# Kernel tuning notes

Hardware: AMD Instinct MI355X
Metric: run time of the kernel (lower is better)

Reference implementation:

```python
import jax, jax.numpy as jnp
import numpy as np

D_MODEL = 1024
NUM_HEADS = 16
D_K = D_MODEL // NUM_HEADS


def setup_inputs() -> dict:
    key = jax.random.key(0)
    ks = jax.random.split(key, 10)
    s = 1.0 / np.sqrt(D_MODEL)  # ~ torch Linear init scale
    inp = {
        "x": jax.random.normal(ks[0], (2, 2048, D_MODEL), dtype=jnp.float32),
        "Wq": jax.random.uniform(ks[1], (D_MODEL, D_MODEL), jnp.float32, -s, s),
        "bq": jax.random.uniform(ks[2], (D_MODEL,), jnp.float32, -s, s),
        "Wk": jax.random.uniform(ks[3], (D_MODEL, D_MODEL), jnp.float32, -s, s),
        "bk": jax.random.uniform(ks[4], (D_MODEL,), jnp.float32, -s, s),
        "Wv": jax.random.uniform(ks[5], (D_MODEL, D_MODEL), jnp.float32, -s, s),
        "bv": jax.random.uniform(ks[6], (D_MODEL,), jnp.float32, -s, s),
        "Wo": jax.random.uniform(ks[7], (D_MODEL, D_MODEL), jnp.float32, -s, s),
        "bo": jax.random.uniform(ks[8], (D_MODEL,), jnp.float32, -s, s),
        "ln_gamma": jnp.ones((D_MODEL,), jnp.float32),
        "ln_beta": jnp.zeros((D_MODEL,), jnp.float32),
    }
    return inp


def reference(x, Wq, bq, Wk, bk, Wv, bv, Wo, bo, ln_gamma, ln_beta):
    B, S, D = x.shape
    residual = x
    # LayerNorm (eps=1e-5 as torch default)
    mu = jnp.mean(x, axis=-1, keepdims=True)
    var = jnp.mean(jnp.square(x - mu), axis=-1, keepdims=True)
    xn = (x - mu) * jax.lax.rsqrt(var + 1e-5) * ln_gamma + ln_beta
    # QKV projections (torch Linear: y = x @ W^T + b) -> (B, H, S, d_k)
    def proj(W, b):
        return (xn @ W.T + b).reshape(B, S, NUM_HEADS, D_K).transpose(0, 2, 1, 3)
    Q, K, V = proj(Wq, bq), proj(Wk, bk), proj(Wv, bv)
    scores = jnp.einsum("bhqd,bhkd->bhqk", Q, K) / np.sqrt(D_K).astype(np.float32)
    attn = jax.nn.softmax(scores, axis=-1)  # (B, H, S, S); dropout is no-op (eval)
    context = jnp.einsum("bhqk,bhkd->bhqd", attn, V)
    context = context.transpose(0, 2, 1, 3).reshape(B, S, D)
    out = context @ Wo.T + bo
    return out + residual, attn.mean(axis=1)
```

## Files before the change

### kernel.cpp

```cpp
#include <hip/hip_runtime.h>
#include <stdint.h>
#include <stddef.h>

#define DEV static __device__ __forceinline__

typedef float f32x4 __attribute__((ext_vector_type(4)));
typedef float f32x16 __attribute__((ext_vector_type(16)));
typedef unsigned u32x4 __attribute__((ext_vector_type(4)));
typedef __bf16 bf16x8 __attribute__((ext_vector_type(8)));

DEV short f2bf(float f) {
  union { float f; unsigned u; } a; a.f = f;
  unsigned r = a.u + 0x7fffu + ((a.u >> 16) & 1u);
  return (short)(r >> 16);
}

DEV void gld_lds16(const void* g, void* lds) {
  __builtin_amdgcn_global_load_lds(
      (__attribute__((address_space(1))) void*)(void*)g,
      (__attribute__((address_space(3))) void*)lds, 16, 0, 0);
}

DEV f32x4 MFMA(bf16x8 a, bf16x8 b, f32x4 c) {
  return __builtin_amdgcn_mfma_f32_16x16x32_bf16(a, b, c, 0, 0, 0);
}
DEV f32x16 MFMA32(bf16x8 a, bf16x8 b, f32x16 c) {
  return __builtin_amdgcn_mfma_f32_32x32x16_bf16(a, b, c, 0, 0, 0);
}

DEV float ex2(float x) { return __builtin_amdgcn_exp2f(x); }

DEV unsigned cvtpk(float lo, float hi) {
  unsigned r;
  asm("v_cvt_pk_bf16_f32 %0, %1, %2" : "=v"(r) : "v"(lo), "v"(hi));
  return r;
}

DEV float xhalf_sum(float v) {
  float a = v, b = v;
  asm volatile("v_permlane32_swap_b32 %0, %1" : "+v"(a), "+v"(b));
  return a + b;
}

#define LOG2E 1.4426950408889634f


__global__ __launch_bounds__(256) void k_cvtw_ln(
    const float* __restrict__ w0, const float* __restrict__ w1,
    const float* __restrict__ w2, const float* __restrict__ w3,
    short* __restrict__ dst, const float* __restrict__ x,
    const float* __restrict__ g, const float* __restrict__ be,
    short* __restrict__ xn) {
  __shared__ float ps[4], pss[4];
  if (blockIdx.x < 4096) {
    int i = blockIdx.x * 256 + threadIdx.x;
    int sel = i >> 18;
    const float* src = sel == 0 ? w0 : sel == 1 ? w1 : sel == 2 ? w2 : w3;
    int off = (i & 0x3ffff) * 4;
    float4 v = *(const float4*)(src + off);
    short4 o4; o4.x = f2bf(v.x); o4.y = f2bf(v.y); o4.z = f2bf(v.z); o4.w = f2bf(v.w);
    *(short4*)(dst + (size_t)i * 4) = o4;
  } else {
    int row = blockIdx.x - 4096;
    int t = threadIdx.x;
    const float4* xr = (const float4*)(x + (size_t)row * 1024);
    float4 v = xr[t];
    float s = v.x + v.y + v.z + v.w;
    float ss = v.x * v.x + v.y * v.y + v.z * v.z + v.w * v.w;
#pragma unroll
    for (int o = 32; o; o >>= 1) { s += __shfl_down(s, o); ss += __shfl_down(ss, o); }
    int w = t >> 6, lane = t & 63;
    if (lane == 0) { ps[w] = s; pss[w] = ss; }
    __syncthreads();
    float st = ps[0] + ps[1] + ps[2] + ps[3];
    float sst = pss[0] + pss[1] + pss[2] + pss[3];
    float mean = st * (1.0f / 1024.0f);
    float var = sst * (1.0f / 1024.0f) - mean * mean;
    float rstd = rsqrtf(var + 1e-5f);
    float4 gv = ((const float4*)g)[t];
    float4 bv = ((const float4*)be)[t];
    short4 o4;
    o4.x = f2bf((v.x - mean) * rstd * gv.x + bv.x);
    o4.y = f2bf((v.y - mean) * rstd * gv.y + bv.y);
    o4.z = f2bf((v.z - mean) * rstd * gv.z + bv.z);
    o4.w = f2bf((v.w - mean) * rstd * gv.w + bv.w);
    ((short4*)(xn + (size_t)row * 1024))[t] = o4;
  }
}

__global__ __launch_bounds__(256) void k_gemm_qkv(
    const short* __restrict__ xn, const short* __restrict__ wbf,
    const float* __restrict__ bq, const float* __restrict__ bk,
    const float* __restrict__ bv, short* __restrict__ q_ws,
    short* __restrict__ k_ws, short* __restrict__ v_ws) {
  __shared__ __align__(16) short at[128 * 32];
  __shared__ __align__(16) short bt[128 * 32];
  int t = threadIdx.x, lane = t & 63, w = t >> 6;
  int wr = w >> 1, wc = w & 1;
  int z = blockIdx.z;
  int row0 = blockIdx.y * 128, col0 = blockIdx.x * 128;
  const short* A = xn + (size_t)row0 * 1024;
  const short* Bw = wbf + (size_t)z * (1024 * 1024) + (size_t)col0 * 1024;
  f32x4 acc[4][4];
#pragma unroll
  for (int m = 0; m < 4; m++)
#pragma unroll
    for (int n = 0; n < 4; n++) acc[m][n] = (f32x4)0.0f;

  for (int k0 = 0; k0 < 1024; k0 += 32) {
#pragma unroll
    for (int i = 0; i < 2; i++) {
      int c = t + i * 256;
      int r = c >> 2, cc = (c & 3) * 8;
      gld_lds16(A + (size_t)r * 1024 + k0 + cc, &at[c * 8]);
      gld_lds16(Bw + (size_t)r * 1024 + k0 + cc, &bt[c * 8]);
    }
    __syncthreads();
    bf16x8 af[4], bfr[4];
#pragma unroll
    for (int m = 0; m < 4; m++)
      af[m] = *(const bf16x8*)&at[(wr * 64 + m * 16 + (lane & 15)) * 32 + (lane >> 4) * 8];
#pragma unroll
    for (int n = 0; n < 4; n++)
      bfr[n] = *(const bf16x8*)&bt[(wc * 64 + n * 16 + (lane & 15)) * 32 + (lane >> 4) * 8];
#pragma unroll
    for (int m = 0; m < 4; m++)
#pragma unroll
      for (int n = 0; n < 4; n++) acc[m][n] = MFMA(af[m], bfr[n], acc[m][n]);
    __syncthreads();
  }
  const float* bias = z == 0 ? bq : z == 1 ? bk : bv;
  short* dst = z == 0 ? q_ws : z == 1 ? k_ws : v_ws;
  float scal = z == 0 ? (0.125f * LOG2E) : 1.0f;
#pragma unroll
  for (int m = 0; m < 4; m++)
#pragma unroll
    for (int n = 0; n < 4; n++)
#pragma unroll
      for (int r = 0; r < 4; r++) {
        int grow = row0 + wr * 64 + m * 16 + (lane >> 4) * 4 + r;
        int gcol = col0 + wc * 64 + n * 16 + (lane & 15);
        float val = (acc[m][n][r] + bias[gcol]) * scal;
        int bb = grow >> 11, s = grow & 2047, h = gcol >> 6, d = gcol & 63;
        dst[(((size_t)bb * 16 + h) * 2048 + s) * 64 + d] = f2bf(val);
      }
}

__global__ __launch_bounds__(256) void k_trv(const short* __restrict__ v_ws,
                                             short* __restrict__ vt_ws) {
  __shared__ short tile[64][65];
  int bh = blockIdx.y, s0 = blockIdx.x * 64;
  const short* src = v_ws + ((size_t)bh * 2048 + s0) * 64;
  int t = threadIdx.x;
#pragma unroll
  for (int i = 0; i < 4; i++) {
    int c = t + i * 256;
    int r = c >> 4, d4 = (c & 15) * 4;
    short4 v4 = *(const short4*)&src[r * 64 + d4];
    tile[d4 + 0][r] = v4.x; tile[d4 + 1][r] = v4.y;
    tile[d4 + 2][r] = v4.z; tile[d4 + 3][r] = v4.w;
  }
  __syncthreads();
#pragma unroll
  for (int i = 0; i < 4; i++) {
    int c = t + i * 256;
    int d = c >> 4, r4 = (c & 15) * 4;
    short4 o4;
    o4.x = tile[d][r4 + 0]; o4.y = tile[d][r4 + 1];
    o4.z = tile[d][r4 + 2]; o4.w = tile[d][r4 + 3];
    *(short4*)&vt_ws[((size_t)bh * 64 + d) * 2048 + s0 + r4] = o4;
  }
}

__global__ __launch_bounds__(256, 2) void k_attn1(
    const short* __restrict__ q_ws, const short* __restrict__ k_ws,
    const short* __restrict__ vt_ws, short* __restrict__ o_ws,
    float* __restrict__ l_ws) {
  __shared__ __align__(16) short k_lds[4][64 * 64];
  __shared__ __align__(16) short vt_lds[4][64 * 64];
  int t = threadIdx.x, lane = t & 63, w = t >> 6;
  int hi = lane >> 5, l31 = lane & 31;
  int qt = blockIdx.x, hd = blockIdx.y, b = blockIdx.z;
  int bh = b * 16 + hd;
  int q0 = qt * 128;
  const short* qb = q_ws + (size_t)bh * (2048 * 64);
  const short* kb = k_ws + (size_t)bh * (2048 * 64);
  const short* vtb = vt_ws + (size_t)bh * (64 * 2048);
  int qg = q0 + w * 32 + l31;

  bf16x8 qf[4];
#pragma unroll
  for (int d4 = 0; d4 < 4; d4++)
    qf[d4] = *(const bf16x8*)&qb[(size_t)qg * 64 + d4 * 16 + hi * 8];
  asm volatile("s_waitcnt vmcnt(0)" ::: "memory");

  const short *kp0, *kp1, *vp0, *vp1;
  {
    int c = t, r = c >> 3, j = (c & 7) ^ (r & 7);
    kp0 = kb + (size_t)r * 64 + j * 8;
    vp0 = vtb + (size_t)r * 2048 + j * 8;
  }
  {
    int c = t + 256, r = c >> 3, j = (c & 7) ^ (r & 7);
    kp1 = kb + (size_t)r * 64 + j * 8;
    vp1 = vtb + (size_t)r * 2048 + j * 8;
  }

  int koff[8];
#pragma unroll
  for (int d4 = 0; d4 < 4; d4++) {
    int row0 = l31, row1 = 32 + l31;
    koff[2 * d4]     = row0 * 64 + (((d4 * 2 + hi) ^ (row0 & 7)) * 8);
    koff[2 * d4 + 1] = row1 * 64 + (((d4 * 2 + hi) ^ (row1 & 7)) * 8);
  }

#define STG(tl_, buf)                                            \
  {                                                              \
    gld_lds16(kp0 + (size_t)(tl_) * 4096, &k_lds[buf][t * 8]);   \
    gld_lds16(kp1 + (size_t)(tl_) * 4096, &k_lds[buf][(t + 256) * 8]); \
    gld_lds16(vp0 + (size_t)(tl_) * 64, &vt_lds[buf][t * 8]);    \
    gld_lds16(vp1 + (size_t)(tl_) * 64, &vt_lds[buf][(t + 256) * 8]); \
  }

  STG(0, 0);
  STG(1, 1);

  f32x16 Oacc[2];
#pragma unroll
  for (int i = 0; i < 16; i++) { Oacc[0][i] = 0.0f; Oacc[1][i] = 0.0f; }
  float lrun = 0.0f;
  bf16x8 pb[4];

  for (int it = 0; it < 32; ++it) {
    int tn = it + 2 <= 31 ? it + 2 : 31;
    STG(tn, (it + 2) & 3);
    asm volatile("s_waitcnt vmcnt(8)" ::: "memory");
    __builtin_amdgcn_s_barrier();

    const short* kl = k_lds[it & 3];
    const short* vl = vt_lds[(it + 3) & 3];

    bf16x8 kfr[8], vfr[8];
#pragma unroll
    for (int i = 0; i < 8; i++) kfr[i] = *(const bf16x8*)&kl[koff[i]];
#pragma unroll
    for (int i = 0; i < 8; i++) vfr[i] = *(const bf16x8*)&vl[koff[i]];

    __builtin_amdgcn_s_setprio(1);
    f32x16 S0 = (f32x16)0.0f, S1 = (f32x16)0.0f;
#pragma unroll
    for (int d4 = 0; d4 < 4; d4++) {
      S0 = MFMA32(kfr[2 * d4], qf[d4], S0);
      S1 = MFMA32(kfr[2 * d4 + 1], qf[d4], S1);
    }
    if (it) {
#pragma unroll
      for (int ks = 0; ks < 4; ks++) {
        Oacc[0] = MFMA32(vfr[2 * ks], pb[ks], Oacc[0]);
        Oacc[1] = MFMA32(vfr[2 * ks + 1], pb[ks], Oacc[1]);
      }
    }
    __builtin_amdgcn_s_setprio(0);

    float rs0 = 0.0f, rs1 = 0.0f;
#pragma unroll
    for (int i = 0; i < 16; i++) {
      float p0 = ex2(S0[i]);
      float p1 = ex2(S1[i]);
      S0[i] = p0; S1[i] = p1;
      rs0 += p0; rs1 += p1;
    }
    lrun += xhalf_sum(rs0 + rs1);

#pragma unroll
    for (int ks = 0; ks < 4; ks++) {
      unsigned wA, wB, wC, wD;
      if (ks == 0) {
        wA = cvtpk(S0[0], S0[1]);  wB = cvtpk(S0[2], S0[3]);
        wC = cvtpk(S0[4], S0[5]);  wD = cvtpk(S0[6], S0[7]);
      } else if (ks == 1) {
        wA = cvtpk(S0[8], S0[9]);  wB = cvtpk(S0[10], S0[11]);
        wC = cvtpk(S0[12], S0[13]); wD = cvtpk(S0[14], S0[15]);
      } else if (ks == 2) {
        wA = cvtpk(S1[0], S1[1]);  wB = cvtpk(S1[2], S1[3]);
        wC = cvtpk(S1[4], S1[5]);  wD = cvtpk(S1[6], S1[7]);
      } else {
        wA = cvtpk(S1[8], S1[9]);  wB = cvtpk(S1[10], S1[11]);
        wC = cvtpk(S1[12], S1[13]); wD = cvtpk(S1[14], S1[15]);
      }
      asm volatile("v_permlane32_swap_b32 %0, %1" : "+v"(wA), "+v"(wC));
      asm volatile("v_permlane32_swap_b32 %0, %1" : "+v"(wB), "+v"(wD));
      u32x4 uu; uu.x = wA; uu.y = wB; uu.z = wC; uu.w = wD;
      pb[ks] = __builtin_bit_cast(bf16x8, uu);
    }
    __builtin_amdgcn_s_barrier();
  }
  asm volatile("s_waitcnt vmcnt(0)" ::: "memory");
  __builtin_amdgcn_s_barrier();

  {
    const short* vl = vt_lds[3];
    __builtin_amdgcn_s_setprio(1);
#pragma unroll
    for (int ks = 0; ks < 4; ks++) {
      Oacc[0] = MFMA32(*(const bf16x8*)&vl[koff[2 * ks]], pb[ks], Oacc[0]);
      Oacc[1] = MFMA32(*(const bf16x8*)&vl[koff[2 * ks + 1]], pb[ks], Oacc[1]);
    }
    __builtin_amdgcn_s_setprio(0);
  }

  float rl = 1.0f / lrun;
  if (lane < 32) {
    l_ws[bh * 2048 + qg] = rl;
  }
#pragma unroll
  for (int dt = 0; dt < 2; dt++)
#pragma unroll
    for (int g = 0; g < 4; g++) {
      short4 o4;
      o4.x = f2bf(Oacc[dt][g * 4 + 0] * rl);
      o4.y = f2bf(Oacc[dt][g * 4 + 1] * rl);
      o4.z = f2bf(Oacc[dt][g * 4 + 2] * rl);
      o4.w = f2bf(Oacc[dt][g * 4 + 3] * rl);
      int d = dt * 32 + g * 8 + hi * 4;
      *(short4*)&o_ws[((size_t)(b * 2048 + qg)) * 1024 + hd * 64 + d] = o4;
    }
}

__global__ __launch_bounds__(256, 3) void k_attn2(
    const short* __restrict__ q_ws, const short* __restrict__ k_ws,
    const float* __restrict__ l_ws, float* __restrict__ out1) {
  __shared__ __align__(16) short q_lds[2][64 * 64];
  __shared__ __align__(16) short k_lds2[2][128 * 64];
  __shared__ __align__(16) float l_lds[2][64];
  int t = threadIdx.x, lane = t & 63, w = t >> 6;
  int k2 = blockIdx.x * 128, q0 = blockIdx.y * 64, b = blockIdx.z;

  f32x4 pacc[8];
#pragma unroll
  for (int n = 0; n < 8; n++) pacc[n] = (f32x4)0.0f;

#define STAGE2(hh, buf)                                                          \
  {                                                                              \
    int bh_ = b * 16 + (hh);                                                     \
    const short* qb_ = q_ws + (size_t)bh_ * (2048 * 64);                         \
    const short* kb_ = k_ws + (size_t)bh_ * (2048 * 64);                         \
    _Pragma("unroll")                                                            \
    for (int i = 0; i < 2; i++) {                                                \
      int c = t + i * 256;                                                       \
      int r = c >> 3, j = (c & 7) ^ (r & 7);                                     \
      gld_lds16(qb_ + (size_t)(q0 + r) * 64 + j * 8, &q_lds[buf][c * 8]);        \
    }                                                                            \
    _Pragma("unroll")                                                            \
    for (int i = 0; i < 4; i++) {                                                \
      int c = t + i * 256;                                                       \
      int r = c >> 3, j = (c & 7) ^ (r & 7);                                     \
      gld_lds16(kb_ + (size_t)(k2 + r) * 64 + j * 8, &k_lds2[buf][c * 8]);       \
    }                                                                            \
    int cc = w * 4 + (t & 63);                                                   \
    if ((t & 63) < 4) {                                                          \
      gld_lds16(&l_ws[(size_t)bh_ * 2048 + q0 + cc * 4], &l_lds[buf][cc * 4]);   \
    }                                                                            \
  }

  STAGE2(0, 0);
  int cur = 0;
  for (int h = 0; h < 16; ++h) {
    int hn = h < 15 ? h + 1 : 15;
    STAGE2(hn, cur ^ 1);
    asm volatile("s_waitcnt vmcnt(7)" ::: "memory");
    __builtin_amdgcn_s_barrier();

    const short* ql = q_lds[cur];
    const short* kl = k_lds2[cur];
    bf16x8 qf[2];
#pragma unroll
    for (int kf = 0; kf < 2; kf++) {
      int row = w * 16 + (lane & 15);
      qf[kf] = *(const bf16x8*)&ql[row * 64 + (((kf * 4 + (lane >> 4)) ^ (row & 7)) * 8)];
    }
    f32x4 sc[8];
#pragma unroll
    for (int n = 0; n < 8; n++) sc[n] = (f32x4)0.0f;
#pragma unroll
    for (int kf = 0; kf < 2; kf++)
#pragma unroll
      for (int n = 0; n < 8; n++) {
        int row = n * 16 + (lane & 15);
        bf16x8 kfr = *(const bf16x8*)&kl[row * 64 + (((kf * 4 + (lane >> 4)) ^ (row & 7)) * 8)];
        sc[n] = MFMA(qf[kf], kfr, sc[n]);
      }
    f32x4 lh = *(const f32x4*)&l_lds[cur][w * 16 + (lane >> 4) * 4];
#pragma unroll
    for (int n = 0; n < 8; n++)
#pragma unroll
      for (int r = 0; r < 4; r++)
        pacc[n][r] += ex2(sc[n][r]) * lh[r];
    __builtin_amdgcn_s_barrier();
    cur ^= 1;
  }

#pragma unroll
  for (int n = 0; n < 8; n++)
#pragma unroll
    for (int r = 0; r < 4; r++) {
      int q = q0 + w * 16 + (lane >> 4) * 4 + r;
      int k = k2 + n * 16 + (lane & 15);
      out1[((size_t)b * 2048 + q) * 2048 + k] = pacc[n][r] * 0.0625f;
    }
}

__global__ __launch_bounds__(256) void k_gemm_out(
    const short* __restrict__ o_ws, const short* __restrict__ wo_bf,
    const float* __restrict__ bo, const float* __restrict__ x,
    float* __restrict__ out0) {
  __shared__ __align__(16) short at[128 * 32];
  __shared__ __align__(16) short bt[128 * 32];
  int t = threadIdx.x, lane = t & 63, w = t >> 6;
  int wr = w >> 1, wc = w & 1;
  int row0 = blockIdx.y * 128, col0 = blockIdx.x * 128;
  const short* A = o_ws + (size_t)row0 * 1024;
  const short* Bw = wo_bf + (size_t)col0 * 1024;
  f32x4 acc[4][4];
#pragma unroll
  for (int m = 0; m < 4; m++)
#pragma unroll
    for (int n = 0; n < 4; n++) acc[m][n] = (f32x4)0.0f;

  for (int k0 = 0; k0 < 1024; k0 += 32) {
#pragma unroll
    for (int i = 0; i < 2; i++) {
      int c = t + i * 256;
      int r = c >> 2, cc = (c & 3) * 8;
      gld_lds16(A + (size_t)r * 1024 + k0 + cc, &at[c * 8]);
      gld_lds16(Bw + (size_t)r * 1024 + k0 + cc, &bt[c * 8]);
    }
    __syncthreads();
    bf16x8 af[4], bfr[4];
#pragma unroll
    for (int m = 0; m < 4; m++)
      af[m] = *(const bf16x8*)&at[(wr * 64 + m * 16 + (lane & 15)) * 32 + (lane >> 4) * 8];
#pragma unroll
    for (int n = 0; n < 4; n++)
      bfr[n] = *(const bf16x8*)&bt[(wc * 64 + n * 16 + (lane & 15)) * 32 + (lane >> 4) * 8];
#pragma unroll
    for (int m = 0; m < 4; m++)
#pragma unroll
      for (int n = 0; n < 4; n++) acc[m][n] = MFMA(af[m], bfr[n], acc[m][n]);
    __syncthreads();
  }
#pragma unroll
  for (int m = 0; m < 4; m++)
#pragma unroll
    for (int n = 0; n < 4; n++)
#pragma unroll
      for (int r = 0; r < 4; r++) {
        int grow = row0 + wr * 64 + m * 16 + (lane >> 4) * 4 + r;
        int gcol = col0 + wc * 64 + n * 16 + (lane & 15);
        float val = acc[m][n][r] + bo[gcol] + x[(size_t)grow * 1024 + gcol];
        out0[(size_t)grow * 1024 + gcol] = val;
      }
}

extern "C" void kernel_launch(void* const* d_in, const int* in_sizes, int n_in,
                              void* d_out, int out_size, void* d_ws, size_t ws_size,
                              hipStream_t stream) {
  (void)in_sizes; (void)n_in; (void)out_size; (void)ws_size;
  const float* x   = (const float*)d_in[0];
  const float* Wq  = (const float*)d_in[1];
  const float* bq  = (const float*)d_in[2];
  const float* Wk  = (const float*)d_in[3];
  const float* bk  = (const float*)d_in[4];
  const float* Wv  = (const float*)d_in[5];
  const float* bv  = (const float*)d_in[6];
  const float* Wo  = (const float*)d_in[7];
  const float* bo  = (const float*)d_in[8];
  const float* lng = (const float*)d_in[9];
  const float* lnb = (const float*)d_in[10];
  float* out0 = (float*)d_out;
  float* out1 = out0 + (size_t)2 * 2048 * 1024;

  char* ws = (char*)d_ws;
  short* xn    = (short*)(ws);
  short* q_ws  = (short*)(ws + 8388608);
  short* k_ws  = (short*)(ws + 16777216);
  short* o_ws  = (short*)(ws + 25165824);
  short* vt_ws = (short*)(ws + 33554432);
  short* wbf   = (short*)(ws + 41943040);
  float* l_ws  = (float*)(ws + 50331648);

  k_cvtw_ln<<<8192, 256, 0, stream>>>(Wq, Wk, Wv, Wo, wbf, x, lng, lnb, xn);
  k_gemm_qkv<<<dim3(8, 32, 3), 256, 0, stream>>>(xn, wbf, bq, bk, bv, q_ws, k_ws, o_ws);
  k_trv<<<dim3(32, 32), 256, 0, stream>>>(o_ws, vt_ws);
  k_attn1<<<dim3(16, 16, 2), 256, 0, stream>>>(q_ws, k_ws, vt_ws, o_ws, l_ws);
  k_attn2<<<dim3(16, 32, 2), 256, 0, stream>>>(q_ws, k_ws, l_ws, out1);
  k_gemm_out<<<dim3(8, 32), 256, 0, stream>>>(o_ws, wbf + (size_t)3 * 1024 * 1024, bo, x, out0);
}
```

Measured before the change: 160.9 us.

## Deepen LDS ring buffers to drop trailing barriers and load Q directly

```diff
diff --git a/kernel.cpp b/kernel.cpp
--- a/kernel.cpp
+++ b/kernel.cpp
@@ -177,7 +177,7 @@
     const short* __restrict__ vt_ws, short* __restrict__ o_ws,
     float* __restrict__ l_ws) {
   __shared__ __align__(16) short k_lds[4][64 * 64];
-  __shared__ __align__(16) short vt_lds[4][64 * 64];
+  __shared__ __align__(16) short vt_lds[5][64 * 64];
   int t = threadIdx.x, lane = t & 63, w = t >> 6;
   int hi = lane >> 5, l31 = lane & 31;
   int qt = blockIdx.x, hd = blockIdx.y, b = blockIdx.z;
@@ -214,16 +214,16 @@
     koff[2 * d4 + 1] = row1 * 64 + (((d4 * 2 + hi) ^ (row1 & 7)) * 8);
   }
 
-#define STG(tl_, buf)                                            \
-  {                                                              \
-    gld_lds16(kp0 + (size_t)(tl_) * 4096, &k_lds[buf][t * 8]);   \
-    gld_lds16(kp1 + (size_t)(tl_) * 4096, &k_lds[buf][(t + 256) * 8]); \
-    gld_lds16(vp0 + (size_t)(tl_) * 64, &vt_lds[buf][t * 8]);    \
-    gld_lds16(vp1 + (size_t)(tl_) * 64, &vt_lds[buf][(t + 256) * 8]); \
-  }
-
-  STG(0, 0);
-  STG(1, 1);
+#define STG(tl_)                                                         \
+  {                                                                      \
+    gld_lds16(kp0 + (size_t)(tl_) * 4096, &k_lds[(tl_) & 3][t * 8]);     \
+    gld_lds16(kp1 + (size_t)(tl_) * 4096, &k_lds[(tl_) & 3][(t + 256) * 8]); \
+    gld_lds16(vp0 + (size_t)(tl_) * 64, &vt_lds[(tl_) % 5][t * 8]);      \
+    gld_lds16(vp1 + (size_t)(tl_) * 64, &vt_lds[(tl_) % 5][(t + 256) * 8]); \
+  }
+
+  STG(0);
+  STG(1);
 
   f32x16 Oacc[2];
 #pragma unroll
@@ -233,12 +233,12 @@
 
   for (int it = 0; it < 32; ++it) {
     int tn = it + 2 <= 31 ? it + 2 : 31;
-    STG(tn, (it + 2) & 3);
+    STG(tn);
     asm volatile("s_waitcnt vmcnt(8)" ::: "memory");
     __builtin_amdgcn_s_barrier();
 
     const short* kl = k_lds[it & 3];
-    const short* vl = vt_lds[(it + 3) & 3];
+    const short* vl = vt_lds[(it + 4) % 5];
 
     bf16x8 kfr[8], vfr[8];
 #pragma unroll
@@ -293,13 +293,12 @@
       u32x4 uu; uu.x = wA; uu.y = wB; uu.z = wC; uu.w = wD;
       pb[ks] = __builtin_bit_cast(bf16x8, uu);
     }
-    __builtin_amdgcn_s_barrier();
   }
   asm volatile("s_waitcnt vmcnt(0)" ::: "memory");
   __builtin_amdgcn_s_barrier();
 
   {
-    const short* vl = vt_lds[3];
+    const short* vl = vt_lds[1];
     __builtin_amdgcn_s_setprio(1);
 #pragma unroll
     for (int ks = 0; ks < 4; ks++) {
@@ -330,9 +329,8 @@
 __global__ __launch_bounds__(256, 3) void k_attn2(
     const short* __restrict__ q_ws, const short* __restrict__ k_ws,
     const float* __restrict__ l_ws, float* __restrict__ out1) {
-  __shared__ __align__(16) short q_lds[2][64 * 64];
-  __shared__ __align__(16) short k_lds2[2][128 * 64];
-  __shared__ __align__(16) float l_lds[2][64];
+  __shared__ __align__(16) short k_lds2[3][128 * 64];
+  __shared__ __align__(16) float l_lds[3][64];
   int t = threadIdx.x, lane = t & 63, w = t >> 6;
   int k2 = blockIdx.x * 128, q0 = blockIdx.y * 64, b = blockIdx.z;
 
@@ -340,45 +338,36 @@
 #pragma unroll
   for (int n = 0; n < 8; n++) pacc[n] = (f32x4)0.0f;
 
-#define STAGE2(hh, buf)                                                          \
+  int qrow = q0 + w * 16 + (lane & 15);
+  size_t qoff0 = (size_t)qrow * 64 + (lane >> 4) * 8;
+  const short* qb0 = q_ws + (size_t)(b * 16) * (2048 * 64);
+
+#define STAGE2(hh)                                                               \
   {                                                                              \
     int bh_ = b * 16 + (hh);                                                     \
-    const short* qb_ = q_ws + (size_t)bh_ * (2048 * 64);                         \
     const short* kb_ = k_ws + (size_t)bh_ * (2048 * 64);                         \
-    _Pragma("unroll")                                                            \
-    for (int i = 0; i < 2; i++) {                                                \
-      int c = t + i * 256;                                                       \
-      int r = c >> 3, j = (c & 7) ^ (r & 7);                                     \
-      gld_lds16(qb_ + (size_t)(q0 + r) * 64 + j * 8, &q_lds[buf][c * 8]);        \
-    }                                                                            \
     _Pragma("unroll")                                                            \
     for (int i = 0; i < 4; i++) {                                                \
       int c = t + i * 256;                                                       \
       int r = c >> 3, j = (c & 7) ^ (r & 7);                                     \
-      gld_lds16(kb_ + (size_t)(k2 + r) * 64 + j * 8, &k_lds2[buf][c * 8]);       \
+      gld_lds16(kb_ + (size_t)(k2 + r) * 64 + j * 8, &k_lds2[(hh) % 3][c * 8]);  \
     }                                                                            \
     int cc = w * 4 + (t & 63);                                                   \
     if ((t & 63) < 4) {                                                          \
-      gld_lds16(&l_ws[(size_t)bh_ * 2048 + q0 + cc * 4], &l_lds[buf][cc * 4]);   \
+      gld_lds16(&l_ws[(size_t)bh_ * 2048 + q0 + cc * 4], &l_lds[(hh) % 3][cc * 4]); \
     }                                                                            \
   }
 
-  STAGE2(0, 0);
-  int cur = 0;
+  STAGE2(0);
   for (int h = 0; h < 16; ++h) {
+    bf16x8 qf0 = *(const bf16x8*)&qb0[(size_t)h * (2048 * 64) + qoff0];
+    bf16x8 qf1 = *(const bf16x8*)&qb0[(size_t)h * (2048 * 64) + qoff0 + 32];
     int hn = h < 15 ? h + 1 : 15;
-    STAGE2(hn, cur ^ 1);
-    asm volatile("s_waitcnt vmcnt(7)" ::: "memory");
+    STAGE2(hn);
+    asm volatile("s_waitcnt vmcnt(5)" ::: "memory");
     __builtin_amdgcn_s_barrier();
 
-    const short* ql = q_lds[cur];
-    const short* kl = k_lds2[cur];
-    bf16x8 qf[2];
-#pragma unroll
-    for (int kf = 0; kf < 2; kf++) {
-      int row = w * 16 + (lane & 15);
-      qf[kf] = *(const bf16x8*)&ql[row * 64 + (((kf * 4 + (lane >> 4)) ^ (row & 7)) * 8)];
-    }
+    const short* kl = k_lds2[h % 3];
     f32x4 sc[8];
 #pragma unroll
     for (int n = 0; n < 8; n++) sc[n] = (f32x4)0.0f;
@@ -388,16 +377,14 @@
       for (int n = 0; n < 8; n++) {
         int row = n * 16 + (lane & 15);
         bf16x8 kfr = *(const bf16x8*)&kl[row * 64 + (((kf * 4 + (lane >> 4)) ^ (row & 7)) * 8)];
-        sc[n] = MFMA(qf[kf], kfr, sc[n]);
+        sc[n] = MFMA(kf == 0 ? qf0 : qf1, kfr, sc[n]);
       }
-    f32x4 lh = *(const f32x4*)&l_lds[cur][w * 16 + (lane >> 4) * 4];
+    f32x4 lh = *(const f32x4*)&l_lds[h % 3][w * 16 + (lane >> 4) * 4];
 #pragma unroll
     for (int n = 0; n < 8; n++)
 #pragma unroll
       for (int r = 0; r < 4; r++)
         pacc[n][r] += ex2(sc[n][r]) * lh[r];
-    __builtin_amdgcn_s_barrier();
-    cur ^= 1;
   }
 
 #pragma unroll
```

After: 160.7 us. Within noise of the previous version (-0.1%).
